# Kernel optimization log

Hardware: AMD Instinct MI355X
Metric: run time of the kernel (lower is better)

Reference implementation:

```python
import jax, jax.numpy as jnp
import numpy as np

B, T, D, V, L = 16, 1024, 512, 5000, 128
BLANK = 0
NEG = -1e30  # log-space 'zero' (avoid inf for stability)


def setup_inputs() -> dict:
    key = jax.random.key(0)
    k1, k2, k3, k4, k5 = jax.random.split(key, 5)
    hs_pad = jax.random.normal(k1, (B, T, D), jnp.float32)
    W = jax.random.normal(k2, (D, V), jnp.float32) * 0.02
    b = jnp.zeros((V,), jnp.float32)
    hlens = jax.random.randint(k3, (B,), T // 2, T + 1)          # frame lengths
    ys_lens = jax.random.randint(k4, (B,), 64, L + 1)             # label lengths
    ys_pad = jax.random.randint(k5, (B, L), 1, V)                 # labels, no blank
    return {"hs_pad": hs_pad, "hlens": hlens, "ys_pad": ys_pad,
            "ys_lens": ys_lens, "W": W, "b": b}


def _lse3(a, b, c):
    m = jnp.maximum(jnp.maximum(a, b), c)
    m = jnp.maximum(m, NEG)
    return m + jnp.log(jnp.exp(a - m) + jnp.exp(b - m) + jnp.exp(c - m))


def _ctc_loss(logp, hlens, ys_pad, ys_lens):
    # logp: (B, T, V) log-probabilities
    Bb, Tt, _ = logp.shape
    Ll = ys_pad.shape[1]
    S = 2 * Ll + 1
    # extended label sequence: blank, y1, blank, y2, ..., blank  -> (B, S)
    ext = jnp.full((Bb, S), BLANK, ys_pad.dtype).at[:, 1::2].set(ys_pad)
    # gather log-probs of extended labels: (B, T, S)
    lp_ext = jnp.take_along_axis(
        logp, jnp.broadcast_to(ext[:, None, :], (Bb, Tt, S)), axis=2)
    # skip transition from s-2 allowed iff ext[s] != blank and ext[s] != ext[s-2]
    ext_m2 = jnp.pad(ext[:, :-2], ((0, 0), (2, 0)), constant_values=-1)
    allow = (ext != BLANK) & (ext != ext_m2)  # (B, S)

    alpha0 = (jnp.full((Bb, S), NEG, logp.dtype)
              .at[:, 0].set(lp_ext[:, 0, 0])
              .at[:, 1].set(lp_ext[:, 0, 1]))

    def step(alpha, xs):
        lp_t, t = xs
        a1 = alpha
        a2 = jnp.pad(alpha[:, :-1], ((0, 0), (1, 0)), constant_values=NEG)
        a3 = jnp.where(allow,
                       jnp.pad(alpha[:, :-2], ((0, 0), (2, 0)), constant_values=NEG),
                       NEG)
        new = _lse3(a1, a2, a3) + lp_t
        keep = (t < hlens)[:, None]  # freeze alpha past each sequence length
        return jnp.where(keep, new, alpha), None

    lp_seq = jnp.swapaxes(lp_ext, 0, 1)  # (T, B, S)
    ts = jnp.arange(1, Tt)
    alpha, _ = jax.lax.scan(step, alpha0, (lp_seq[1:], ts))

    idx1 = 2 * ys_lens                 # final blank
    idx2 = jnp.maximum(idx1 - 1, 0)    # final label
    a_end = jnp.take_along_axis(alpha, jnp.stack([idx1, idx2], axis=1), axis=1)
    ll = jax.scipy.special.logsumexp(a_end, axis=1)  # (B,)
    loss = -ll
    loss = jnp.where(jnp.isfinite(loss) & (loss < 1e29), loss, 0.0)  # zero_infinity
    # reduction='sum', then normalize by total token count (normalize_length=True)
    return jnp.sum(loss) / jnp.sum(ys_lens).astype(logp.dtype)


def reference(hs_pad, hlens, ys_pad, ys_lens, W, b):
    logits = hs_pad @ W + b                      # (B, T, V), dropout_rate=0
    logp = jax.nn.log_softmax(logits, axis=2)    # same math as transpose->log_softmax
    return _ctc_loss(logp, hlens, ys_pad, ys_lens)
```

## Files before the change

### kernel.cpp

```cpp
#include <hip/hip_runtime.h>
#include <hip/hip_bf16.h>
#include <math.h>

#define B_   16
#define T_   1024
#define D_   512
#define V_   5000
#define VP_  5120
#define L_   128
#define S_   257
#define J_   129
#define JP_  160
#define M_   (B_*T_)
#define NT_  40
#define NEGF (-1e30f)
#define LOG2E_F 1.4426950408889634f

typedef __attribute__((ext_vector_type(8))) short short8;
typedef __attribute__((ext_vector_type(4))) float float4v;

__device__ inline void load_lds_16(const void* g, void* l) {
    __builtin_amdgcn_global_load_lds(
        (const __attribute__((address_space(1))) unsigned int*)g,
        (__attribute__((address_space(3))) unsigned int*)l, 16, 0, 0);
}

__device__ inline unsigned short f2bf(float f) {
    union { float f; unsigned int u; } x; x.f = f;
    unsigned int r = x.u + 0x7FFFu + ((x.u >> 16) & 1u);
    return (unsigned short)(r >> 16);
}

__device__ inline float wave_shr1_f32(float v) {
    return __int_as_float(__builtin_amdgcn_update_dpp(
        0, __float_as_int(v), 0x138, 0xF, 0xF, true));
}
__device__ inline int wave_shr1_i32(int v) {
    return __builtin_amdgcn_update_dpp(0, v, 0x138, 0xF, 0xF, true);
}

__global__ __launch_bounds__(256) void k_convert_hs(
    const float* __restrict__ hs, unsigned short* __restrict__ Ah)
{
    size_t base = ((size_t)blockIdx.x * 256 + threadIdx.x) * 8;
    float4 a = *(const float4*)&hs[base];
    float4 b = *(const float4*)&hs[base + 4];
    short8 o;
    o[0] = (short)f2bf(a.x); o[1] = (short)f2bf(a.y);
    o[2] = (short)f2bf(a.z); o[3] = (short)f2bf(a.w);
    o[4] = (short)f2bf(b.x); o[5] = (short)f2bf(b.y);
    o[6] = (short)f2bf(b.z); o[7] = (short)f2bf(b.w);
    *(short8*)&Ah[base] = o;
}

__global__ __launch_bounds__(256) void k_transpose_w(
    const float* __restrict__ W, unsigned short* __restrict__ Wt)
{
    __shared__ float tile[32][33];
    int v0 = blockIdx.x * 32, k0 = blockIdx.y * 32;
    int tx = threadIdx.x, ty = threadIdx.y;
#pragma unroll
    for (int r = 0; r < 4; r++) {
        int kk = r * 8 + ty;
        float val = 0.f;
        if (v0 + tx < V_) val = W[(size_t)(k0 + kk) * V_ + v0 + tx];
        tile[kk][tx] = val;
    }
    __syncthreads();
#pragma unroll
    for (int r = 0; r < 4; r++) {
        int vloc = r * 8 + ty;
        Wt[(size_t)(v0 + vloc) * D_ + k0 + tx] = f2bf(tile[tx][vloc]);
    }
}

__global__ __launch_bounds__(256) void k_gemm_lse_mfma(
    const unsigned short* __restrict__ Ah,
    const unsigned short* __restrict__ Wt,
    const float* __restrict__ bias,
    float* __restrict__ part_s)
{
    __shared__ unsigned short As[128 * 32];
    __shared__ unsigned short Bs[128 * 32];
    __shared__ float sm_s[2][128];

    const int bx = blockIdx.x;
    const int by = blockIdx.y;
    const int tid = threadIdx.x;
    const int rowBase = bx * 128, colBase = by * 128;
    const int lane = tid & 63, wv = tid >> 6;
    const int wi = wv >> 1, wj = wv & 1;
    const int g = lane >> 4, lo = lane & 15;
    const int cs = g ^ (lo & 3);

    float4v acc[4][4];
#pragma unroll
    for (int i = 0; i < 4; i++)
#pragma unroll
        for (int j = 0; j < 4; j++) acc[i][j] = (float4v){0.f, 0.f, 0.f, 0.f};

    for (int it = 0; it < 16; it++) {
        const int k0 = it * 32;
        __syncthreads();
#pragma unroll
        for (int l = 0; l < 2; l++) {
            int slot = tid + l * 256;
            int r = slot >> 2, q = slot & 3;
            int qs = q ^ (r & 3);
            load_lds_16(&Ah[(size_t)(rowBase + r) * D_ + k0 + qs * 8],
                        &As[r * 32 + q * 8]);
            load_lds_16(&Wt[(size_t)(colBase + r) * D_ + k0 + qs * 8],
                        &Bs[r * 32 + q * 8]);
        }
        __syncthreads();

        short8 a[4], b[4];
#pragma unroll
        for (int i = 0; i < 4; i++)
            a[i] = *(const short8*)&As[(wi * 64 + i * 16 + lo) * 32 + cs * 8];
#pragma unroll
        for (int j = 0; j < 4; j++)
            b[j] = *(const short8*)&Bs[(wj * 64 + j * 16 + lo) * 32 + cs * 8];
#pragma unroll
        for (int i = 0; i < 4; i++)
#pragma unroll
            for (int j = 0; j < 4; j++)
                acc[i][j] = __builtin_amdgcn_mfma_f32_16x16x32_bf16(
                    a[i], b[j], acc[i][j], 0, 0, 0);
    }

    float bj[4]; bool vj[4];
#pragma unroll
    for (int j = 0; j < 4; j++) {
        int col = colBase + wj * 64 + j * 16 + lo;
        vj[j] = (col < V_);
        bj[j] = vj[j] ? bias[col] : 0.f;
    }
#pragma unroll
    for (int i = 0; i < 4; i++) {
#pragma unroll
        for (int r = 0; r < 4; r++) {
            float s = 0.f;
#pragma unroll
            for (int j = 0; j < 4; j++)
                if (vj[j]) s += __expf(acc[i][j][r] + bj[j]);
#pragma unroll
            for (int off = 1; off < 16; off <<= 1)
                s += __shfl_xor(s, off, 16);
            if (lo == 0)
                sm_s[wj][wi * 64 + i * 16 + g * 4 + r] = s;
        }
    }
    __syncthreads();
    if (tid < 128)
        part_s[(size_t)(rowBase + tid) * NT_ + by] = sm_s[0][tid] + sm_s[1][tid];
}

__global__ __launch_bounds__(64) void k_gather_wb(
    const unsigned short* __restrict__ Wt,
    const float* __restrict__ bias,
    const int* __restrict__ ys,
    unsigned short* __restrict__ Wgb,
    float* __restrict__ bgb)
{
    int b = blockIdx.x, j = blockIdx.y;
    int lab = 0;
    if (j >= 1 && j <= L_) lab = ys[b * L_ + (j - 1)];
    else if (j > L_) lab = VP_ - 1;
    const unsigned short* src = &Wt[(size_t)lab * D_];
    unsigned short* dst = &Wgb[((size_t)b * JP_ + j) * D_];
    int t = threadIdx.x;
    *(short8*)&dst[t * 8] = *(const short8*)&src[t * 8];
    if (t == 0) bgb[b * JP_ + j] = (j <= L_) ? bias[lab] : 0.f;
}

__global__ __launch_bounds__(256) void k_label_mfma(
    const unsigned short* __restrict__ Ah,
    const unsigned short* __restrict__ Wgb,
    const float* __restrict__ bgb,
    const float* __restrict__ part_s,
    float* __restrict__ ll,
    float* __restrict__ lb2)
{
    __shared__ unsigned short As[64 * 32];
    __shared__ unsigned short Bs[JP_ * 32];
    __shared__ float outs[64][JP_ + 1];

    const int b = blockIdx.x, t0 = blockIdx.y * 64;
    const int tid = threadIdx.x;
    const int lane = tid & 63, w = tid >> 6;
    const int g = lane >> 4, lo = lane & 15;

    const unsigned short* Ab = Ah  + ((size_t)b * T_ + t0) * D_;
    const unsigned short* Bb = Wgb + (size_t)b * JP_ * D_;

    float4v acc[10];
#pragma unroll
    for (int j = 0; j < 10; j++) acc[j] = (float4v){0.f, 0.f, 0.f, 0.f};

    for (int it = 0; it < 16; it++) {
        const int k0 = it * 32;
        __syncthreads();
        {
            int r = tid >> 2, q = tid & 3;
            load_lds_16(&Ab[(size_t)r * D_ + k0 + q * 8], &As[r * 32 + q * 8]);
        }
        for (int s = tid; s < 640; s += 256) {
            int r = s >> 2, q = s & 3;
            load_lds_16(&Bb[(size_t)r * D_ + k0 + q * 8], &Bs[r * 32 + q * 8]);
        }
        __syncthreads();

        short8 a = *(const short8*)&As[(w * 16 + lo) * 32 + g * 8];
#pragma unroll
        for (int j = 0; j < 10; j++) {
            short8 bf = *(const short8*)&Bs[(j * 16 + lo) * 32 + g * 8];
            acc[j] = __builtin_amdgcn_mfma_f32_16x16x32_bf16(a, bf, acc[j], 0, 0, 0);
        }
    }

#pragma unroll
    for (int j = 0; j < 10; j++) {
        float bv = bgb[b * JP_ + j * 16 + lo];
#pragma unroll
        for (int r = 0; r < 4; r++)
            outs[w * 16 + g * 4 + r][j * 16 + lo] = acc[j][r] + bv;
    }
    __syncthreads();
    for (int idx = tid; idx < 64 * J_; idx += 256) {
        int r = idx / J_, j = idx - r * J_;
        float l0 = outs[r][0];
        float v  = outs[r][j];
        ll[((size_t)b * T_ + t0 + r) * J_ + j] = (j == 0) ? 1.f : __expf(v - l0);
    }
    if (tid < 64) {
        size_t row = (size_t)b * T_ + t0 + tid;
        const float* ps = &part_s[row * NT_];
        float s = 0.f;
#pragma unroll
        for (int i = 0; i < NT_; i++) s += ps[i];
        lb2[row] = (outs[tid][0] - __logf(s)) * LOG2E_F;
    }
}

#define CH_   32
#define CHB_  (CH_ * J_ * 4)
#define NLD_  ((CHB_ + 1023) / 1024)

__global__ __launch_bounds__(64, 1) void k_ctc_alpha(
    const float* __restrict__ Pr,
    const float* __restrict__ lb2,
    const int* __restrict__ hlens,
    const int* __restrict__ ys,
    const int* __restrict__ ys_lens,
    float* __restrict__ loss_b)
{
    __shared__ float llds[2][NLD_ * 256];
    __shared__ float fin_m[S_];
    __shared__ int   fin_e[S_];
    const int b = blockIdx.x;
    const int l = threadIdx.x;
    const int hl = hlens[b];
    const float* prb = Pr  + (size_t)b * T_ * J_;
    const float* lbb = lb2 + (size_t)b * T_;

    double acc = 0.0;
    for (int tt = l; tt < hl; tt += 64) acc += (double)lbb[tt];
#pragma unroll
    for (int off = 32; off > 0; off >>= 1)
        acc += __shfl_xor(acc, off, 64);

    float u1f = 0.f, u3f;
    {
        const int* yb = ys + b * L_;
        if (l >= 1) u1f = (yb[2 * l] != yb[2 * l - 1]) ? 1.f : 0.f;
        u3f = (yb[2 * l + 1] != yb[2 * l]) ? 1.f : 0.f;
    }
    const int c1 = 2 * l + 1;

    float a0 = (l == 0) ? 1.f : 0.f;
    float a1 = (l == 0) ? prb[1] : 0.f;
    float a2 = 0.f, a3 = 0.f, a4 = 0.f;
    int   E  = 0;
    float fl   = (l == 0) ? 0.f : 1.f;
    float u1fl = u1f * fl;

#define RENORM() do {                                                         \
        float mx_ = fmaxf(fmaxf(fmaxf(a0, a1), fmaxf(a2, a3)), a4);           \
        unsigned long long act_ = __ballot(mx_ > 0.f);                        \
        int La_ = 63 - __builtin_clzll(act_);           \
        if (mx_ > 0.f) {                                                      \
            int e_ = (int)((__float_as_uint(mx_) >> 23) & 255u) - 127;        \
            a0 = ldexpf(a0, -e_); a1 = ldexpf(a1, -e_); a2 = ldexpf(a2, -e_); \
            a3 = ldexpf(a3, -e_); a4 = ldexpf(a4, -e_);                       \
            E += e_;                                                          \
        }                                                                     \
        int Ea_ = __shfl(E, La_, 64);                                         \
        if (!(mx_ > 0.f)) E = Ea_;                   \
        int Ep_ = wave_shr1_i32(E);                                           \
        int dE_ = Ep_ - E;                                                    \
        dE_ = dE_ > 126 ? 126 : (dE_ < -126 ? -126 : dE_);                    \
        fl = (l == 0) ? 0.f : ldexpf(1.f, dE_);                               \
        u1fl = u1f * fl;                                                      \
    } while (0)

#define STEP(r_) do {                                                         \
        float p1_ = lbuf[(r_) * J_ + c1];                                     \
        float p3_ = lbuf[(r_) * J_ + c1 + 1];                                 \
        float prev_ = wave_shr1_f32(a3);                                      \
        float n0_ = fmaf(prev_, fl, a0);                                      \
        float n1_ = fmaf(prev_, u1fl, a0 + a1) * p1_;                         \
        float n2_ = a2 + a1;                                                  \
        float n3_ = fmaf(a1, u3f, a3 + a2) * p3_;                             \
        float n4_ = a4 + a3;                                                  \
        a0 = n0_; a1 = n1_; a2 = n2_; a3 = n3_; a4 = n4_;                     \
    } while (0)

    {
        const char* src = (const char*)prb;
        char* dst = (char*)&llds[0][0];
#pragma unroll
        for (int k = 0; k < NLD_; k++)
            load_lds_16(src + (size_t)k * 1024 + (size_t)l * 16, dst + k * 1024);
    }

    const int nch = (hl + CH_ - 1) / CH_;
    int t = 1;
    for (int c = 0; c < nch; c++) {
        asm volatile("s_waitcnt vmcnt(0)" ::: "memory");
        __builtin_amdgcn_sched_barrier(0);
        if (c + 1 < nch) {
            const char* src = (const char*)(prb + (size_t)(c + 1) * CH_ * J_);
            char* dst = (char*)&llds[(c + 1) & 1][0];
#pragma unroll
            for (int k = 0; k < NLD_; k++)
                load_lds_16(src + (size_t)k * 1024 + (size_t)l * 16, dst + k * 1024);
        }
        const float* lbuf = &llds[c & 1][0];
        const int cbase = c * CH_;
        const int tcap = (hl < cbase + CH_) ? hl : cbase + CH_;
        const int tmid = (tcap < cbase + 16) ? tcap : cbase + 16;
#pragma unroll 8
        for (; t < tmid; t++) STEP(t - cbase);
        RENORM();
#pragma unroll 8
        for (; t < tcap; t++) STEP(t - cbase);
        RENORM();
    }

    fin_m[4 * l + 0] = a0; fin_m[4 * l + 1] = a1;
    fin_m[4 * l + 2] = a2; fin_m[4 * l + 3] = a3;
    fin_e[4 * l + 0] = E;  fin_e[4 * l + 1] = E;
    fin_e[4 * l + 2] = E;  fin_e[4 * l + 3] = E;
    if (l == 63) { fin_m[256] = a4; fin_e[256] = E; }
    __syncthreads();

    if (l == 0) {
        int yl = ys_lens[b];
        int i1 = 2 * yl;
        int i2 = (i1 > 0) ? i1 - 1 : 0;
        int Ea = fin_e[i1], Eb = fin_e[i2];
        int Em = Ea > Eb ? Ea : Eb;
        int da = Ea - Em, db = Eb - Em;
        da = da < -126 ? -126 : da;  db = db < -126 ? -126 : db;
        float v = ldexpf(fin_m[i1], da) + ldexpf(fin_m[i2], db);
        float lg = __log2f(v) + (float)Em;
        double lln = ((double)lg + acc) * 0.6931471805599453;
        float loss = -(float)lln;
        if (!isfinite(loss) || loss >= 1e29f) loss = 0.f;
        loss_b[b] = loss;
    }
#undef RENORM
#undef STEP
}

__global__ void k_final(const float* __restrict__ loss_b,
                        const int* __restrict__ ys_lens,
                        float* __restrict__ out)
{
    int t = threadIdx.x;
    float v = (t < B_) ? loss_b[t] : 0.f;
    int   n = (t < B_) ? ys_lens[t] : 0;
    for (int off = 32; off > 0; off >>= 1) {
        v += __shfl_down(v, off, 64);
        n += __shfl_down(n, off, 64);
    }
    if (t == 0) out[0] = v / (float)n;
}

extern "C" void kernel_launch(void* const* d_in, const int* in_sizes, int n_in,
                              void* d_out, int out_size, void* d_ws, size_t ws_size,
                              hipStream_t stream)
{
    const float* hs      = (const float*)d_in[0];
    const int*   hlens   = (const int*)  d_in[1];
    const int*   ys      = (const int*)  d_in[2];
    const int*   ys_lens = (const int*)  d_in[3];
    const float* W       = (const float*)d_in[4];
    const float* bias    = (const float*)d_in[5];
    float* out = (float*)d_out;

    float* ws = (float*)d_ws;
    float* part_s = ws;
    unsigned short* Wgb = (unsigned short*)(part_s + (size_t)M_ * NT_);
    float* bgb    = (float*)(Wgb + (size_t)B_ * JP_ * D_);
    float* llab   = bgb    + (size_t)B_ * JP_;
    float* loss_b = llab   + (size_t)B_ * T_ * J_;
    float* lb2    = loss_b + 16;
    unsigned short* Ah = (unsigned short*)(lb2 + M_);
    unsigned short* Wt = Ah + (size_t)M_ * D_;

    k_convert_hs<<<(M_ * D_) / (256 * 8), 256, 0, stream>>>(hs, Ah);
    k_transpose_w<<<dim3(VP_ / 32, D_ / 32), dim3(32, 8), 0, stream>>>(W, Wt);
    k_gemm_lse_mfma<<<dim3(M_ / 128, NT_), 256, 0, stream>>>(Ah, Wt, bias, part_s);
    k_gather_wb<<<dim3(B_, JP_), 64, 0, stream>>>(Wt, bias, ys, Wgb, bgb);
    k_label_mfma<<<dim3(B_, T_ / 64), 256, 0, stream>>>(Ah, Wgb, bgb, part_s, llab, lb2);
    k_ctc_alpha<<<B_, 64, 0, stream>>>(llab, lb2, hlens, ys, ys_lens, loss_b);
    k_final<<<1, 64, 0, stream>>>(loss_b, ys_lens, out);
}
```

Before: 290.7 us.

## Enlarge GEMM row tile to 256 with 512 threads and batch CTC LDS loads

The logits GEMM block now covers 256 rows with 8 waves instead of 128 rows with 4 waves. Each W tile loaded into LDS is therefore reused across twice as many rows, which halves W traffic per output and halves the grid size. In the CTC alpha recursion, the per-step LDS reads of label log-probs are hoisted into groups of 8 ahead of the dependent arithmetic, so LDS latency can overlap with the serial chain. The costs are fewer blocks (fewer waves to hide latency per CU) and more registers in the alpha loop.

```diff
diff --git a/kernel.cpp b/kernel.cpp
--- a/kernel.cpp
+++ b/kernel.cpp
@@ -74,20 +74,20 @@
     }
 }
 
-__global__ __launch_bounds__(256) void k_gemm_lse_mfma(
+__global__ __launch_bounds__(512) void k_gemm_lse_mfma(
     const unsigned short* __restrict__ Ah,
     const unsigned short* __restrict__ Wt,
     const float* __restrict__ bias,
     float* __restrict__ part_s)
 {
-    __shared__ unsigned short As[128 * 32];
+    __shared__ unsigned short As[256 * 32];
     __shared__ unsigned short Bs[128 * 32];
-    __shared__ float sm_s[2][128];
+    __shared__ float sm_s[2][256];
 
     const int bx = blockIdx.x;
     const int by = blockIdx.y;
     const int tid = threadIdx.x;
-    const int rowBase = bx * 128, colBase = by * 128;
+    const int rowBase = bx * 256, colBase = by * 128;
     const int lane = tid & 63, wv = tid >> 6;
     const int wi = wv >> 1, wj = wv & 1;
     const int g = lane >> 4, lo = lane & 15;
@@ -103,14 +103,20 @@
         const int k0 = it * 32;
         __syncthreads();
 #pragma unroll
-        for (int l = 0; l < 2; l++) {
-            int slot = tid + l * 256;
-            int r = slot >> 2, q = slot & 3;
-            int qs = q ^ (r & 3);
-            load_lds_16(&Ah[(size_t)(rowBase + r) * D_ + k0 + qs * 8],
-                        &As[r * 32 + q * 8]);
-            load_lds_16(&Wt[(size_t)(colBase + r) * D_ + k0 + qs * 8],
-                        &Bs[r * 32 + q * 8]);
+        for (int l = 0; l < 3; l++) {
+            int slot = tid + l * 512;
+            if (slot < 1024) {
+                int r = slot >> 2, q = slot & 3;
+                int qs = q ^ (r & 3);
+                load_lds_16(&Ah[(size_t)(rowBase + r) * D_ + k0 + qs * 8],
+                            &As[r * 32 + q * 8]);
+            } else {
+                int s = slot - 1024;
+                int r = s >> 2, q = s & 3;
+                int qs = q ^ (r & 3);
+                load_lds_16(&Wt[(size_t)(colBase + r) * D_ + k0 + qs * 8],
+                            &Bs[r * 32 + q * 8]);
+            }
         }
         __syncthreads();
 
@@ -152,7 +158,7 @@
         }
     }
     __syncthreads();
-    if (tid < 128)
+    if (tid < 256)
         part_s[(size_t)(rowBase + tid) * NT_ + by] = sm_s[0][tid] + sm_s[1][tid];
 }
 
@@ -304,14 +310,12 @@
         u1fl = u1f * fl;                                                      \
     } while (0)
 
-#define STEP(r_) do {                                                         \
-        float p1_ = lbuf[(r_) * J_ + c1];                                     \
-        float p3_ = lbuf[(r_) * J_ + c1 + 1];                                 \
+#define STEP_P(p1_, p3_) do {                                                 \
         float prev_ = wave_shr1_f32(a3);                                      \
         float n0_ = fmaf(prev_, fl, a0);                                      \
-        float n1_ = fmaf(prev_, u1fl, a0 + a1) * p1_;                         \
+        float n1_ = fmaf(prev_, u1fl, a0 + a1) * (p1_);                       \
         float n2_ = a2 + a1;                                                  \
-        float n3_ = fmaf(a1, u3f, a3 + a2) * p3_;                             \
+        float n3_ = fmaf(a1, u3f, a3 + a2) * (p3_);                           \
         float n4_ = a4 + a3;                                                  \
         a0 = n0_; a1 = n1_; a2 = n2_; a3 = n3_; a4 = n4_;                     \
     } while (0)
@@ -340,12 +344,30 @@
         const int cbase = c * CH_;
         const int tcap = (hl < cbase + CH_) ? hl : cbase + CH_;
         const int tmid = (tcap < cbase + 16) ? tcap : cbase + 16;
-#pragma unroll 8
-        for (; t < tmid; t++) STEP(t - cbase);
-        RENORM();
-#pragma unroll 8
-        for (; t < tcap; t++) STEP(t - cbase);
-        RENORM();
+#pragma unroll
+        for (int half = 0; half < 2; half++) {
+            const int tlim = (half == 0) ? tmid : tcap;
+            while (t + 8 <= tlim) {
+                float pv1[8], pv3[8];
+#pragma unroll
+                for (int i = 0; i < 8; i++) {
+                    int r = t + i - cbase;
+                    pv1[i] = lbuf[r * J_ + c1];
+                    pv3[i] = lbuf[r * J_ + c1 + 1];
+                }
+#pragma unroll
+                for (int i = 0; i < 8; i++) STEP_P(pv1[i], pv3[i]);
+                t += 8;
+            }
+            while (t < tlim) {
+                int r = t - cbase;
+                float p1 = lbuf[r * J_ + c1];
+                float p3 = lbuf[r * J_ + c1 + 1];
+                STEP_P(p1, p3);
+                t++;
+            }
+            RENORM();
+        }
     }
 
     fin_m[4 * l + 0] = a0; fin_m[4 * l + 1] = a1;
@@ -371,7 +393,7 @@
         loss_b[b] = loss;
     }
 #undef RENORM
-#undef STEP
+#undef STEP_P
 }
 
 __global__ void k_final(const float* __restrict__ loss_b,
@@ -412,7 +434,7 @@
 
     k_convert_hs<<<(M_ * D_) / (256 * 8), 256, 0, stream>>>(hs, Ah);
     k_transpose_w<<<dim3(VP_ / 32, D_ / 32), dim3(32, 8), 0, stream>>>(W, Wt);
-    k_gemm_lse_mfma<<<dim3(M_ / 128, NT_), 256, 0, stream>>>(Ah, Wt, bias, part_s);
+    k_gemm_lse_mfma<<<dim3(M_ / 256, NT_), 512, 0, stream>>>(Ah, Wt, bias, part_s);
     k_gather_wb<<<dim3(B_, JP_), 64, 0, stream>>>(Wt, bias, ys, Wgb, bgb);
     k_label_mfma<<<dim3(B_, T_ / 64), 256, 0, stream>>>(Ah, Wgb, bgb, part_s, llab, lb2);
     k_ctc_alpha<<<B_, 64, 0, stream>>>(llab, lb2, hlens, ys, ys_lens, loss_b);
```

Result: faster. 263.0 us (-9.5%).
